# Kernel optimization log

Measured on AMD Instinct MI355X. Metric: run time of the kernel, lower is better.

Reference implementation:

```python
import jax, jax.numpy as jnp
import numpy as np

TEMPERATURE = 0.07
EPS_NORM = 1e-12  # F.normalize eps

def _l2_normalize(x):
    # matches torch.nn.functional.normalize(dim=1): x / max(||x||, eps)
    norm = jnp.linalg.norm(x, axis=1, keepdims=True)
    return x / jnp.maximum(norm, EPS_NORM)

def setup_inputs() -> dict:
    key = jax.random.key(0)
    k1, k2, k3, k4 = jax.random.split(key, 4)
    N, M, D, C = 8192, 8192, 1024, 128
    return {
        "features_a": jax.random.normal(k1, (N, D), dtype=jnp.float32),
        "features_b": jax.random.normal(k2, (M, D), dtype=jnp.float32),
        "labels_a": jax.random.randint(k3, (N,), 0, C, dtype=jnp.int64),
        "labels_b": jax.random.randint(k4, (M,), 0, C, dtype=jnp.int64),
    }

def reference(features_a, features_b, labels_a, labels_b):
    fa = _l2_normalize(features_a)
    fb = _l2_normalize(features_b)
    sim = jnp.matmul(fa, fb.T) / TEMPERATURE          # [N, M]
    sim = jnp.clip(sim, -50.0, 50.0)
    exp_sim = jnp.exp(sim)
    positive_mask = (labels_a[:, None] == labels_b[None, :]).astype(exp_sim.dtype)
    pos_sum = jnp.sum(exp_sim * positive_mask, axis=1, keepdims=True)
    neg_sum = jnp.sum(exp_sim, axis=1, keepdims=True)
    pos_sum = jnp.maximum(pos_sum, 1e-8)
    loss = -jnp.mean(jnp.log(pos_sum / neg_sum))
    return loss
```

## Files before the change

### kernel.cpp

```cpp
#include <hip/hip_runtime.h>
#include <hip/hip_bf16.h>
#include <math.h>

typedef __attribute__((ext_vector_type(4))) float f32x4;
typedef __attribute__((ext_vector_type(16))) float f32x16;
typedef __attribute__((ext_vector_type(8))) int i32x8;
typedef __attribute__((ext_vector_type(4))) int i32x4;

#define TEMP_INV 14.2857142857142857f
#define SCALE_EPI 0.013950892857142857f
#define UNIT_SCALE 0x7f7f7f7f

union frag32 {
  i32x8 v8;
  struct { i32x4 lo; i32x4 hi; } s;
};

static __device__ inline void async16(const void* g, void* l) {
  __builtin_amdgcn_global_load_lds(
      (const __attribute__((address_space(1))) unsigned int*)g,
      (__attribute__((address_space(3))) unsigned int*)l,
      16, 0, 0);
}

static __device__ inline int fp4e(float y) {
  const float af = fabsf(y);
  int code = (af > 0.25f) + (af > 0.75f) + (af > 1.25f) + (af > 1.75f) +
             (af > 2.5f) + (af > 3.5f) + (af > 5.0f);
  return code | (y < 0.f ? 8 : 0);
}


__global__ __launch_bounds__(1024) void normalize_rows(
    const float* __restrict__ a, const float* __restrict__ b,
    int* __restrict__ oa, int* __restrict__ ob,
    float* __restrict__ pos_acc, float* __restrict__ neg_acc,
    int N, int D) {
  __shared__ __align__(16) unsigned short sPk[8192];

  const int blk = blockIdx.x;
  const bool isA = blk < 256;
  const int p = isA ? blk : blk - 256;
  const float* src = (isA ? a : b) + (size_t)p * 32 * D;
  int* out = isA ? oa : ob;

  const int tid = threadIdx.x;
  const int r = tid >> 5;
  const int c = tid & 31;

  if (isA && c == 0) {
    pos_acc[p * 32 + r] = 0.f;
    neg_acc[p * 32 + r] = 0.f;
  }

  const float4* inr = (const float4*)(src + (size_t)r * D);
  float4 v[8];
#pragma unroll
  for (int i = 0; i < 8; i++) v[i] = inr[c + 32 * i];

  float ss = 0.f;
#pragma unroll
  for (int i = 0; i < 8; i++)
    ss += v[i].x * v[i].x + v[i].y * v[i].y + v[i].z * v[i].z + v[i].w * v[i].w;
#pragma unroll
  for (int m = 16; m >= 1; m >>= 1) ss += __shfl_xor(ss, m, 32);
  const float inv = 32.0f / fmaxf(sqrtf(ss), 1e-12f);

#pragma unroll
  for (int i = 0; i < 8; i++) {
    const int f = c + 32 * i;
    const int n0 = fp4e(v[i].x * inv);
    const int n1 = fp4e(v[i].y * inv);
    const int n2 = fp4e(v[i].z * inv);
    const int n3 = fp4e(v[i].w * inv);
    const unsigned short h =
        (unsigned short)(n0 | (n1 << 4) | (n2 << 8) | (n3 << 12));
    const int s = f >> 4;
    const int hi = (f >> 3) & 1;
    sPk[s * 512 + (hi * 32 + r) * 8 + (f & 7)] = h;
  }
  __syncthreads();

  const int4* sp4 = (const int4*)sPk;
  ((int4*)out)[(size_t)p * 1024 + tid] = sp4[tid];
}

__global__ __launch_bounds__(256, 4) void infonce_gemm(
    const unsigned char* __restrict__ A, const unsigned char* __restrict__ B,
    const int* __restrict__ la, const int* __restrict__ lb,
    float* __restrict__ pos_acc, float* __restrict__ neg_acc) {
  __shared__ __align__(16) unsigned char sA[16384];
  __shared__ __align__(16) unsigned char sB[16384];

  const int tid = threadIdx.x;
  const int lane = tid & 63;
  const int wave = tid >> 6;
  const int wm = wave >> 1;
  const int wn = wave & 1;

  const int bid = blockIdx.x;
  const int xcd = bid & 7;
  const int local = bid >> 3;
  const int by = xcd * 8 + (local & 7);
  const int bx = local >> 3;
  const int row0 = by * 128;
  const int col0 = bx * 128;

  const unsigned char* gA =
      A + (size_t)by * 65536 + ((tid >> 6) & 3) * 1024 + (tid & 63) * 16;
  const unsigned char* gB =
      B + (size_t)bx * 65536 + ((tid >> 6) & 3) * 1024 + (tid & 63) * 16;

  f32x16 acc[2][2] = {};

#define STAGE(kt)                                                   \
  do {                                                              \
    _Pragma("unroll") for (int u = 0; u < 4; u++) {                 \
      async16(gA + (size_t)u * 16384 + (size_t)(kt)*4096,           \
              &sA[u * 4096 + tid * 16]);                            \
      async16(gB + (size_t)u * 16384 + (size_t)(kt)*4096,           \
              &sB[u * 4096 + tid * 16]);                            \
    }                                                               \
  } while (0)

#define LD16(dst, base, off)                                        \
  do {                                                              \
    frag32 _f;                                                      \
    _f.s.lo = *(const i32x4*)((base) + (off));                      \
    _f.s.hi = (i32x4){0, 0, 0, 0};                                  \
    dst = _f.v8;                                                    \
  } while (0)

#define MFMA(ci, a_, b_)                                            \
  ci = __builtin_amdgcn_mfma_scale_f32_32x32x64_f8f6f4(             \
      a_, b_, ci, 4, 4, 0, UNIT_SCALE, 0, UNIT_SCALE)

  const int lofs = lane * 16;
  const int aoff0 = (wm * 2 + 0) * 4096 + lofs;
  const int aoff1 = (wm * 2 + 1) * 4096 + lofs;
  const int boff0 = (wn * 2 + 0) * 4096 + lofs;
  const int boff1 = (wn * 2 + 1) * 4096 + lofs;

#pragma unroll 1
  for (int kt = 0; kt < 4; ++kt) {
    STAGE(kt);
    __syncthreads();
#pragma unroll
    for (int sp = 0; sp < 4; ++sp) {
      i32x8 fa0, fa1, fb0, fb1;
      LD16(fa0, sA, aoff0 + sp * 1024);
      LD16(fa1, sA, aoff1 + sp * 1024);
      LD16(fb0, sB, boff0 + sp * 1024);
      LD16(fb1, sB, boff1 + sp * 1024);
      MFMA(acc[0][0], fa0, fb0);
      MFMA(acc[0][1], fa0, fb1);
      MFMA(acc[1][0], fa1, fb0);
      MFMA(acc[1][1], fa1, fb1);
    }
    __syncthreads();
  }

  const int l31 = lane & 31;
  const int hi = lane >> 5;
  const int lb0 = lb[col0 + wn * 64 + l31];
  const int lb1 = lb[col0 + wn * 64 + 32 + l31];
  const int rbase = row0 + wm * 64 + 4 * hi;
  const int rfin = rbase + (l31 & 3) + 8 * ((l31 >> 2) & 3);
  const int bb0 = l31 & 1, bb1 = (l31 >> 1) & 1, bb2 = (l31 >> 2) & 1,
            bb3 = (l31 >> 3) & 1;

#pragma unroll
  for (int mi = 0; mi < 2; mi++) {
    float vn[16], vp[16];
#pragma unroll
    for (int r = 0; r < 16; r++) {
      const int row = rbase + mi * 32 + (r & 3) + 8 * (r >> 2);
      const int lav = la[row];
      const float e0 = __expf(acc[mi][0][r] * SCALE_EPI);
      const float e1 = __expf(acc[mi][1][r] * SCALE_EPI);
      vn[r] = e0 + e1;
      vp[r] = (lav == lb0 ? e0 : 0.f) + (lav == lb1 ? e1 : 0.f);
    }
    float an[8], ap[8];
#pragma unroll
    for (int t = 0; t < 8; t++) {
      float sn = bb0 ? vn[2 * t] : vn[2 * t + 1];
      float sp = bb0 ? vp[2 * t] : vp[2 * t + 1];
      float kn = bb0 ? vn[2 * t + 1] : vn[2 * t];
      float kp = bb0 ? vp[2 * t + 1] : vp[2 * t];
      an[t] = kn + __shfl_xor(sn, 1, 64);
      ap[t] = kp + __shfl_xor(sp, 1, 64);
    }
    float cn[4], cp[4];
#pragma unroll
    for (int t = 0; t < 4; t++) {
      float sn = bb1 ? an[2 * t] : an[2 * t + 1];
      float sp = bb1 ? ap[2 * t] : ap[2 * t + 1];
      float kn = bb1 ? an[2 * t + 1] : an[2 * t];
      float kp = bb1 ? ap[2 * t + 1] : ap[2 * t];
      cn[t] = kn + __shfl_xor(sn, 2, 64);
      cp[t] = kp + __shfl_xor(sp, 2, 64);
    }
    float dn[2], dp[2];
#pragma unroll
    for (int t = 0; t < 2; t++) {
      float sn = bb2 ? cn[2 * t] : cn[2 * t + 1];
      float sp = bb2 ? cp[2 * t] : cp[2 * t + 1];
      float kn = bb2 ? cn[2 * t + 1] : cn[2 * t];
      float kp = bb2 ? cp[2 * t + 1] : cp[2 * t];
      dn[t] = kn + __shfl_xor(sn, 4, 64);
      dp[t] = kp + __shfl_xor(sp, 4, 64);
    }
    float sn4 = bb3 ? dn[0] : dn[1];
    float sp4 = bb3 ? dp[0] : dp[1];
    float fn = (bb3 ? dn[1] : dn[0]) + __shfl_xor(sn4, 8, 64);
    float fp = (bb3 ? dp[1] : dp[0]) + __shfl_xor(sp4, 8, 64);
    fn += __shfl_xor(fn, 16, 64);
    fp += __shfl_xor(fp, 16, 64);
    if (l31 < 16) {
      const int row = rfin + mi * 32;
      atomicAdd(&neg_acc[row], fn);
      atomicAdd(&pos_acc[row], fp);
    }
  }
}

__global__ __launch_bounds__(1024) void final_reduce(
    const float* __restrict__ pos, const float* __restrict__ neg,
    float* __restrict__ out, int N) {
  double local = 0.0;
  const int t = threadIdx.x;
  for (int i = t; i < N / 4; i += 1024) {
    const float4 p4 = ((const float4*)pos)[i];
    const float4 n4 = ((const float4*)neg)[i];
    local += (double)(logf(n4.x) - logf(fmaxf(p4.x, 1e-8f)));
    local += (double)(logf(n4.y) - logf(fmaxf(p4.y, 1e-8f)));
    local += (double)(logf(n4.z) - logf(fmaxf(p4.z, 1e-8f)));
    local += (double)(logf(n4.w) - logf(fmaxf(p4.w, 1e-8f)));
  }
#pragma unroll
  for (int m = 32; m >= 1; m >>= 1) local += __shfl_xor(local, m, 64);
  __shared__ double wsum[16];
  const int wave = t >> 6, lane = t & 63;
  if (lane == 0) wsum[wave] = local;
  __syncthreads();
  if (t == 0) {
    double tot = 0.0;
#pragma unroll
    for (int w = 0; w < 16; w++) tot += wsum[w];
    out[0] = (float)(tot / (double)N);
  }
}

extern "C" void kernel_launch(void* const* d_in, const int* in_sizes, int n_in,
                              void* d_out, int out_size, void* d_ws, size_t ws_size,
                              hipStream_t stream) {
  const float* fa = (const float*)d_in[0];
  const float* fb = (const float*)d_in[1];
  const int* la = (const int*)d_in[2];
  const int* lb = (const int*)d_in[3];

  const int D = 1024;
  const int N = in_sizes[0] / D;
  const int M = in_sizes[1] / D;

  unsigned char* nA = (unsigned char*)d_ws;
  unsigned char* nB = nA + (size_t)N * D / 2;
  float* pos = (float*)(nB + (size_t)M * D / 2);
  float* neg = pos + N;

  normalize_rows<<<512, 1024, 0, stream>>>(fa, fb, (int*)nA, (int*)nB, pos,
                                           neg, N, D);

  infonce_gemm<<<4096, 256, 0, stream>>>(nA, nB, la, lb, pos, neg);

  final_reduce<<<1, 1024, 0, stream>>>(pos, neg, (float*)d_out, N);
}
```

Measured before the change: 155.6 us.

## Swap MFMA operands so rows map to lanes and parallelize final reduction

The MFMA operands are swapped so each lane's accumulator holds one A row across many B columns. The per-row sums can then be done in registers with a single cross-half shuffle instead of a multi-stage butterfly of selects and shuffles. B labels are preloaded per lane. The final reduction now runs over 8 blocks that atomically add into an output zeroed by the normalize kernel, using float instead of double accumulation. This may add small rounding differences and makes the result order-nondeterministic.

```diff
diff --git a/kernel.cpp b/kernel.cpp
--- a/kernel.cpp
+++ b/kernel.cpp
@@ -35,7 +35,7 @@
     const float* __restrict__ a, const float* __restrict__ b,
     int* __restrict__ oa, int* __restrict__ ob,
     float* __restrict__ pos_acc, float* __restrict__ neg_acc,
-    int N, int D) {
+    float* __restrict__ dout, int N, int D) {
   __shared__ __align__(16) unsigned short sPk[8192];
 
   const int blk = blockIdx.x;
@@ -48,6 +48,7 @@
   const int r = tid >> 5;
   const int c = tid & 31;
 
+  if (blk == 0 && tid == 0) dout[0] = 0.f;
   if (isA && c == 0) {
     pos_acc[p * 32 + r] = 0.f;
     neg_acc[p * 32 + r] = 0.f;
@@ -95,8 +96,8 @@
   const int tid = threadIdx.x;
   const int lane = tid & 63;
   const int wave = tid >> 6;
-  const int wm = wave >> 1;
-  const int wn = wave & 1;
+  const int wa = wave >> 1;
+  const int wb = wave & 1;
 
   const int bid = blockIdx.x;
   const int xcd = bid & 7;
@@ -131,15 +132,15 @@
     dst = _f.v8;                                                    \
   } while (0)
 
-#define MFMA(ci, a_, b_)                                            \
+#define MFMA(ci, x_, y_)                                            \
   ci = __builtin_amdgcn_mfma_scale_f32_32x32x64_f8f6f4(             \
-      a_, b_, ci, 4, 4, 0, UNIT_SCALE, 0, UNIT_SCALE)
+      x_, y_, ci, 4, 4, 0, UNIT_SCALE, 0, UNIT_SCALE)
 
   const int lofs = lane * 16;
-  const int aoff0 = (wm * 2 + 0) * 4096 + lofs;
-  const int aoff1 = (wm * 2 + 1) * 4096 + lofs;
-  const int boff0 = (wn * 2 + 0) * 4096 + lofs;
-  const int boff1 = (wn * 2 + 1) * 4096 + lofs;
+  const int aoff0 = (wa * 2 + 0) * 4096 + lofs;
+  const int aoff1 = (wa * 2 + 1) * 4096 + lofs;
+  const int boff0 = (wb * 2 + 0) * 4096 + lofs;
+  const int boff1 = (wb * 2 + 1) * 4096 + lofs;
 
 #pragma unroll 1
   for (int kt = 0; kt < 4; ++kt) {
@@ -152,104 +153,69 @@
       LD16(fa1, sA, aoff1 + sp * 1024);
       LD16(fb0, sB, boff0 + sp * 1024);
       LD16(fb1, sB, boff1 + sp * 1024);
-      MFMA(acc[0][0], fa0, fb0);
-      MFMA(acc[0][1], fa0, fb1);
-      MFMA(acc[1][0], fa1, fb0);
-      MFMA(acc[1][1], fa1, fb1);
+      MFMA(acc[0][0], fb0, fa0);
+      MFMA(acc[0][1], fb0, fa1);
+      MFMA(acc[1][0], fb1, fa0);
+      MFMA(acc[1][1], fb1, fa1);
     }
     __syncthreads();
   }
 
   const int l31 = lane & 31;
   const int hi = lane >> 5;
-  const int lb0 = lb[col0 + wn * 64 + l31];
-  const int lb1 = lb[col0 + wn * 64 + 32 + l31];
-  const int rbase = row0 + wm * 64 + 4 * hi;
-  const int rfin = rbase + (l31 & 3) + 8 * ((l31 >> 2) & 3);
-  const int bb0 = l31 & 1, bb1 = (l31 >> 1) & 1, bb2 = (l31 >> 2) & 1,
-            bb3 = (l31 >> 3) & 1;
-
-#pragma unroll
-  for (int mi = 0; mi < 2; mi++) {
-    float vn[16], vp[16];
-#pragma unroll
-    for (int r = 0; r < 16; r++) {
-      const int row = rbase + mi * 32 + (r & 3) + 8 * (r >> 2);
-      const int lav = la[row];
-      const float e0 = __expf(acc[mi][0][r] * SCALE_EPI);
-      const float e1 = __expf(acc[mi][1][r] * SCALE_EPI);
-      vn[r] = e0 + e1;
-      vp[r] = (lav == lb0 ? e0 : 0.f) + (lav == lb1 ? e1 : 0.f);
+  const int colw = col0 + wb * 64 + 4 * hi;
+  const int rowbase = row0 + wa * 64 + l31;
+
+  const int lav0 = la[rowbase];
+  const int lav1 = la[rowbase + 32];
+
+  int lbs[2][16];
+#pragma unroll
+  for (int bi = 0; bi < 2; bi++)
+#pragma unroll
+    for (int r = 0; r < 16; r++)
+      lbs[bi][r] = lb[colw + bi * 32 + (r & 3) + 8 * (r >> 2)];
+
+#pragma unroll
+  for (int aj = 0; aj < 2; aj++) {
+    const int lav = aj ? lav1 : lav0;
+    float sn = 0.f, sp = 0.f;
+#pragma unroll
+    for (int bi = 0; bi < 2; bi++)
+#pragma unroll
+      for (int r = 0; r < 16; r++) {
+        const float e = __expf(acc[bi][aj][r] * SCALE_EPI);
+        sn += e;
+        sp += (lav == lbs[bi][r]) ? e : 0.f;
+      }
+    sn += __shfl_xor(sn, 32, 64);
+    sp += __shfl_xor(sp, 32, 64);
+    if (hi == 0) {
+      const int row = rowbase + aj * 32;
+      atomicAdd(&neg_acc[row], sn);
+      atomicAdd(&pos_acc[row], sp);
     }
-    float an[8], ap[8];
-#pragma unroll
-    for (int t = 0; t < 8; t++) {
-      float sn = bb0 ? vn[2 * t] : vn[2 * t + 1];
-      float sp = bb0 ? vp[2 * t] : vp[2 * t + 1];
-      float kn = bb0 ? vn[2 * t + 1] : vn[2 * t];
-      float kp = bb0 ? vp[2 * t + 1] : vp[2 * t];
-      an[t] = kn + __shfl_xor(sn, 1, 64);
-      ap[t] = kp + __shfl_xor(sp, 1, 64);
-    }
-    float cn[4], cp[4];
-#pragma unroll
-    for (int t = 0; t < 4; t++) {
-      float sn = bb1 ? an[2 * t] : an[2 * t + 1];
-      float sp = bb1 ? ap[2 * t] : ap[2 * t + 1];
-      float kn = bb1 ? an[2 * t + 1] : an[2 * t];
-      float kp = bb1 ? ap[2 * t + 1] : ap[2 * t];
-      cn[t] = kn + __shfl_xor(sn, 2, 64);
-      cp[t] = kp + __shfl_xor(sp, 2, 64);
-    }
-    float dn[2], dp[2];
-#pragma unroll
-    for (int t = 0; t < 2; t++) {
-      float sn = bb2 ? cn[2 * t] : cn[2 * t + 1];
-      float sp = bb2 ? cp[2 * t] : cp[2 * t + 1];
-      float kn = bb2 ? cn[2 * t + 1] : cn[2 * t];
-      float kp = bb2 ? cp[2 * t + 1] : cp[2 * t];
-      dn[t] = kn + __shfl_xor(sn, 4, 64);
-      dp[t] = kp + __shfl_xor(sp, 4, 64);
-    }
-    float sn4 = bb3 ? dn[0] : dn[1];
-    float sp4 = bb3 ? dp[0] : dp[1];
-    float fn = (bb3 ? dn[1] : dn[0]) + __shfl_xor(sn4, 8, 64);
-    float fp = (bb3 ? dp[1] : dp[0]) + __shfl_xor(sp4, 8, 64);
-    fn += __shfl_xor(fn, 16, 64);
-    fp += __shfl_xor(fp, 16, 64);
-    if (l31 < 16) {
-      const int row = rfin + mi * 32;
-      atomicAdd(&neg_acc[row], fn);
-      atomicAdd(&pos_acc[row], fp);
-    }
-  }
-}
-
-__global__ __launch_bounds__(1024) void final_reduce(
+  }
+}
+
+__global__ __launch_bounds__(256) void final_reduce(
     const float* __restrict__ pos, const float* __restrict__ neg,
     float* __restrict__ out, int N) {
-  double local = 0.0;
-  const int t = threadIdx.x;
-  for (int i = t; i < N / 4; i += 1024) {
-    const float4 p4 = ((const float4*)pos)[i];
-    const float4 n4 = ((const float4*)neg)[i];
-    local += (double)(logf(n4.x) - logf(fmaxf(p4.x, 1e-8f)));
-    local += (double)(logf(n4.y) - logf(fmaxf(p4.y, 1e-8f)));
-    local += (double)(logf(n4.z) - logf(fmaxf(p4.z, 1e-8f)));
-    local += (double)(logf(n4.w) - logf(fmaxf(p4.w, 1e-8f)));
-  }
+  const int i = blockIdx.x * 256 + threadIdx.x;
+  const float4 p4 = ((const float4*)pos)[i];
+  const float4 n4 = ((const float4*)neg)[i];
+  float local = (logf(n4.x) - logf(fmaxf(p4.x, 1e-8f))) +
+                (logf(n4.y) - logf(fmaxf(p4.y, 1e-8f))) +
+                (logf(n4.z) - logf(fmaxf(p4.z, 1e-8f))) +
+                (logf(n4.w) - logf(fmaxf(p4.w, 1e-8f)));
 #pragma unroll
   for (int m = 32; m >= 1; m >>= 1) local += __shfl_xor(local, m, 64);
-  __shared__ double wsum[16];
-  const int wave = t >> 6, lane = t & 63;
-  if (lane == 0) wsum[wave] = local;
+  __shared__ float ws[4];
+  const int wv = threadIdx.x >> 6, lane = threadIdx.x & 63;
+  if (lane == 0) ws[wv] = local;
   __syncthreads();
-  if (t == 0) {
-    double tot = 0.0;
-#pragma unroll
-    for (int w = 0; w < 16; w++) tot += wsum[w];
-    out[0] = (float)(tot / (double)N);
-  }
+  if (threadIdx.x == 0)
+    atomicAdd(out, (ws[0] + ws[1] + ws[2] + ws[3]) * (1.0f / (float)N));
 }
 
 extern "C" void kernel_launch(void* const* d_in, const int* in_sizes, int n_in,
@@ -270,9 +236,9 @@
   float* neg = pos + N;
 
   normalize_rows<<<512, 1024, 0, stream>>>(fa, fb, (int*)nA, (int*)nB, pos,
-                                           neg, N, D);
+                                           neg, (float*)d_out, N, D);
 
   infonce_gemm<<<4096, 256, 0, stream>>>(nA, nB, la, lb, pos, neg);
 
-  final_reduce<<<1, 1024, 0, stream>>>(pos, neg, (float*)d_out, N);
-}
+  final_reduce<<<8, 256, 0, stream>>>(pos, neg, (float*)d_out, N);
+}
```

Result: faster. 148.1 us (-4.8%).
